# Kernel tuning notes

Hardware: AMD Instinct MI355X
Metric: run time of the kernel (lower is better)

The kernel has to match this reference:

```python
import jax, jax.numpy as jnp
import numpy as np

# Physical constants (normalized units, CFL-stable: c*dt/dx = 0.5)
DX = 0.01
DT = 0.005
C = 1.0
EPSILON = 1.0

def _make_kernels():
    # D02: second derivative along last axis (x); D20 = transpose (y)
    d02 = np.array([[0.0, 0.0, 0.0],
                    [1.0, -2.0, 1.0],
                    [0.0, 0.0, 0.0]], dtype=np.float32) / (DX * DX)
    d20 = d02.T
    # OIHW, single in/out channel
    return jnp.asarray(d02)[None, None], jnp.asarray(d20)[None, None]

_D02, _D20 = _make_kernels()

def _conv3x3(u, k):
    # same padding, stride 1, NCHW
    return jax.lax.conv_general_dilated(
        u, k, window_strides=(1, 1), padding=[(1, 1), (1, 1)],
        dimension_numbers=('NCHW', 'OIHW', 'NCHW'))

def setup_inputs() -> dict:
    key = jax.random.key(0)
    k1, k2, k3, k4 = jax.random.split(key, 4)
    B, H, W = 16, 1024, 1024
    shp = (B, 1, H, W)
    return {
        'u1': jax.random.normal(k1, shp, dtype=jnp.float32),
        'u0': jax.random.normal(k2, shp, dtype=jnp.float32),
        'j2': jax.random.normal(k3, shp, dtype=jnp.float32),
        'j0': jax.random.normal(k4, shp, dtype=jnp.float32),
    }

def reference(u1, u0, j2, j0):
    D20u1 = _conv3x3(u1, _D20)  # d^2/dy^2
    D02u1 = _conv3x3(u1, _D02)  # d^2/dx^2
    u2 = (2.0 * u1 - u0
          + (DT * DT) * (C * C) * (D20u1 + D02u1)
          - (DT / (2.0 * EPSILON)) * (j2 - j0))
    return u2
```

## Files before the change

### kernel.cpp

```cpp
#include <hip/hip_runtime.h>

#define WIDTH  1024
#define HEIGHT 1024

typedef float vfloat4 __attribute__((ext_vector_type(4)));

__global__ __launch_bounds__(256) void fdtd_kernel(
    const float* __restrict__ u1,
    const float* __restrict__ u0,
    const float* __restrict__ j2,
    const float* __restrict__ j0,
    float* __restrict__ out,
    int rowsplit)
{
    const int row = blockIdx.x;
    const int y   = row & (HEIGHT - 1);
    const int x0  = threadIdx.x << 2;
    const vfloat4 zero = {0.f, 0.f, 0.f, 0.f};

    long base[2];
    base[0] = (long)row * WIDTH + x0;
    base[1] = base[0] + (long)rowsplit * WIDTH;

    vfloat4 c[2], up[2], dn[2], a0[2], v2[2], v0[2];
    float   lf[2], rt[2];
#pragma unroll
    for (int k = 0; k < 2; ++k) {
        const long b = base[k];
        c[k]  = *(const vfloat4*)(u1 + b);
        up[k] = (y > 0)          ? *(const vfloat4*)(u1 + b - WIDTH) : zero;
        dn[k] = (y < HEIGHT - 1) ? *(const vfloat4*)(u1 + b + WIDTH) : zero;
        a0[k] = __builtin_nontemporal_load((const vfloat4*)(u0 + b));
        v2[k] = __builtin_nontemporal_load((const vfloat4*)(j2 + b));
        v0[k] = __builtin_nontemporal_load((const vfloat4*)(j0 + b));
        lf[k] = (x0 > 0)         ? u1[b - 1] : 0.0f;
        rt[k] = (x0 + 4 < WIDTH) ? u1[b + 4] : 0.0f;
    }

#pragma unroll
    for (int k = 0; k < 2; ++k) {
        vfloat4 o;
        o.x = 2.0f * c[k].x - a0[k].x + 0.25f * (up[k].x + dn[k].x + lf[k]   + c[k].y - 4.0f * c[k].x)
            - 0.0025f * (v2[k].x - v0[k].x);
        o.y = 2.0f * c[k].y - a0[k].y + 0.25f * (up[k].y + dn[k].y + c[k].x  + c[k].z - 4.0f * c[k].y)
            - 0.0025f * (v2[k].y - v0[k].y);
        o.z = 2.0f * c[k].z - a0[k].z + 0.25f * (up[k].z + dn[k].z + c[k].y  + c[k].w - 4.0f * c[k].z)
            - 0.0025f * (v2[k].z - v0[k].z);
        o.w = 2.0f * c[k].w - a0[k].w + 0.25f * (up[k].w + dn[k].w + c[k].z  + rt[k]  - 4.0f * c[k].w)
            - 0.0025f * (v2[k].w - v0[k].w);
        __builtin_nontemporal_store(o, (vfloat4*)(out + base[k]));
    }
}

extern "C" void kernel_launch(void* const* d_in, const int* in_sizes, int n_in,
                              void* d_out, int out_size, void* d_ws, size_t ws_size,
                              hipStream_t stream) {
    const float* u1 = (const float*)d_in[0];
    const float* u0 = (const float*)d_in[1];
    const float* j2 = (const float*)d_in[2];
    const float* j0 = (const float*)d_in[3];
    float* out = (float*)d_out;

    const int nrows = out_size / WIDTH;
    const int rowsplit = nrows / 2;
    dim3 block(WIDTH / 4);
    dim3 grid(rowsplit);
    fdtd_kernel<<<grid, block, 0, stream>>>(u1, u0, j2, j0, out, rowsplit);
}
```

Before: 246.7 us.

## Process four consecutive rows per block with register reuse and XCD-aware block swizzle

Each block now handles four adjacent rows, so the centre rows of u1 held in registers double as the up/down neighbours of adjacent rows and vertical halo loads drop from three per row to about one and a half. Block IDs are also swizzled so that blocks dispatched round-robin across the eight chiplets map to contiguous row ranges, which should improve L2 locality for halo rows. The trade-offs are more registers per thread and a grid with half as many blocks.

```diff
diff --git a/kernel.cpp b/kernel.cpp
--- a/kernel.cpp
+++ b/kernel.cpp
@@ -2,6 +2,7 @@
 
 #define WIDTH  1024
 #define HEIGHT 1024
+#define R      4
 
 typedef float vfloat4 __attribute__((ext_vector_type(4)));
 
@@ -11,44 +12,53 @@
     const float* __restrict__ j2,
     const float* __restrict__ j0,
     float* __restrict__ out,
-    int rowsplit)
+    int chunk)
 {
-    const int row = blockIdx.x;
-    const int y   = row & (HEIGHT - 1);
-    const int x0  = threadIdx.x << 2;
+    const int bid = blockIdx.x;
+    const int swz = chunk ? ((bid & 7) * chunk + (bid >> 3)) : bid;
+
+    const int y0 = swz * R;
+    const int iy = y0 & (HEIGHT - 1);
+    const int x0 = threadIdx.x << 2;
+    const long base = (long)y0 * WIDTH + x0;
     const vfloat4 zero = {0.f, 0.f, 0.f, 0.f};
 
-    long base[2];
-    base[0] = (long)row * WIDTH + x0;
-    base[1] = base[0] + (long)rowsplit * WIDTH;
+    vfloat4 c[R + 2];
+    c[0] = (iy > 0) ? *(const vfloat4*)(u1 + base - WIDTH) : zero;
+#pragma unroll
+    for (int r = 0; r < R; ++r)
+        c[r + 1] = *(const vfloat4*)(u1 + base + (long)r * WIDTH);
+    c[R + 1] = (iy + R < HEIGHT) ? *(const vfloat4*)(u1 + base + (long)R * WIDTH) : zero;
 
-    vfloat4 c[2], up[2], dn[2], a0[2], v2[2], v0[2];
-    float   lf[2], rt[2];
+    float lf[R], rt[R];
 #pragma unroll
-    for (int k = 0; k < 2; ++k) {
-        const long b = base[k];
-        c[k]  = *(const vfloat4*)(u1 + b);
-        up[k] = (y > 0)          ? *(const vfloat4*)(u1 + b - WIDTH) : zero;
-        dn[k] = (y < HEIGHT - 1) ? *(const vfloat4*)(u1 + b + WIDTH) : zero;
-        a0[k] = __builtin_nontemporal_load((const vfloat4*)(u0 + b));
-        v2[k] = __builtin_nontemporal_load((const vfloat4*)(j2 + b));
-        v0[k] = __builtin_nontemporal_load((const vfloat4*)(j0 + b));
-        lf[k] = (x0 > 0)         ? u1[b - 1] : 0.0f;
-        rt[k] = (x0 + 4 < WIDTH) ? u1[b + 4] : 0.0f;
+    for (int r = 0; r < R; ++r) {
+        lf[r] = (x0 > 0)         ? u1[base + (long)r * WIDTH - 1] : 0.f;
+        rt[r] = (x0 + 4 < WIDTH) ? u1[base + (long)r * WIDTH + 4] : 0.f;
+    }
+
+    vfloat4 a0[R], v2[R], v0[R];
+#pragma unroll
+    for (int r = 0; r < R; ++r) {
+        const long b = base + (long)r * WIDTH;
+        a0[r] = __builtin_nontemporal_load((const vfloat4*)(u0 + b));
+        v2[r] = __builtin_nontemporal_load((const vfloat4*)(j2 + b));
+        v0[r] = __builtin_nontemporal_load((const vfloat4*)(j0 + b));
     }
 
 #pragma unroll
-    for (int k = 0; k < 2; ++k) {
+    for (int r = 0; r < R; ++r) {
+        const vfloat4 up = c[r], ce = c[r + 1], dn = c[r + 2];
         vfloat4 o;
-        o.x = 2.0f * c[k].x - a0[k].x + 0.25f * (up[k].x + dn[k].x + lf[k]   + c[k].y - 4.0f * c[k].x)
-            - 0.0025f * (v2[k].x - v0[k].x);
-        o.y = 2.0f * c[k].y - a0[k].y + 0.25f * (up[k].y + dn[k].y + c[k].x  + c[k].z - 4.0f * c[k].y)
-            - 0.0025f * (v2[k].y - v0[k].y);
-        o.z = 2.0f * c[k].z - a0[k].z + 0.25f * (up[k].z + dn[k].z + c[k].y  + c[k].w - 4.0f * c[k].z)
-            - 0.0025f * (v2[k].z - v0[k].z);
-        o.w = 2.0f * c[k].w - a0[k].w + 0.25f * (up[k].w + dn[k].w + c[k].z  + rt[k]  - 4.0f * c[k].w)
-            - 0.0025f * (v2[k].w - v0[k].w);
-        __builtin_nontemporal_store(o, (vfloat4*)(out + base[k]));
+        o.x = 2.0f * ce.x - a0[r].x + 0.25f * (up.x + dn.x + lf[r] + ce.y - 4.0f * ce.x)
+            - 0.0025f * (v2[r].x - v0[r].x);
+        o.y = 2.0f * ce.y - a0[r].y + 0.25f * (up.y + dn.y + ce.x + ce.z - 4.0f * ce.y)
+            - 0.0025f * (v2[r].y - v0[r].y);
+        o.z = 2.0f * ce.z - a0[r].z + 0.25f * (up.z + dn.z + ce.y + ce.w - 4.0f * ce.z)
+            - 0.0025f * (v2[r].z - v0[r].z);
+        o.w = 2.0f * ce.w - a0[r].w + 0.25f * (up.w + dn.w + ce.z + rt[r] - 4.0f * ce.w)
+            - 0.0025f * (v2[r].w - v0[r].w);
+        __builtin_nontemporal_store(o, (vfloat4*)(out + base + (long)r * WIDTH));
     }
 }
 
@@ -61,9 +71,11 @@
     const float* j0 = (const float*)d_in[3];
     float* out = (float*)d_out;
 
-    const int nrows = out_size / WIDTH;
-    const int rowsplit = nrows / 2;
+    const int nrows   = out_size / WIDTH;
+    const int nblocks = nrows / R;
+    const int chunk   = (nblocks % 8 == 0) ? (nblocks >> 3) : 0;
+
     dim3 block(WIDTH / 4);
-    dim3 grid(rowsplit);
-    fdtd_kernel<<<grid, block, 0, stream>>>(u1, u0, j2, j0, out, rowsplit);
+    dim3 grid(nblocks);
+    fdtd_kernel<<<grid, block, 0, stream>>>(u1, u0, j2, j0, out, chunk);
 }
```

Measured after the change: 247.3 us. No clear change (+0.2%).
